# Performance work log

Measured on AMD Instinct MI355X. Metric: run time of the kernel, lower is better.

The kernel has to match this reference:

```python
import jax, jax.numpy as jnp
import numpy as np

N_HEAD = 16

def setup_inputs() -> dict:
    key = jax.random.key(0)
    ks = jax.random.split(key, 5)
    B, T, C = 2, 2048, 1024
    s = 0.02
    return {
        "x": jax.random.normal(ks[0], (B, T, C), jnp.float32),
        "W_attn": jax.random.normal(ks[1], (3 * C, C), jnp.float32) * s,
        "b_attn": jax.random.normal(ks[2], (3 * C,), jnp.float32) * s,
        "W_proj": jax.random.normal(ks[3], (C, C), jnp.float32) * s,
        "b_proj": jax.random.normal(ks[4], (C,), jnp.float32) * s,
    }

def reference(x, W_attn, b_attn, W_proj, b_proj):
    B, T, C = x.shape
    H = N_HEAD
    D = C // H
    # fused QKV projection (torch Linear: y = x @ W.T + b)
    qkv = jnp.einsum('btc,fc->btf', x, W_attn) + b_attn  # [B,T,3C]
    q, k, v = jnp.split(qkv, 3, axis=-1)
    def to_heads(t):
        return t.reshape(B, T, H, D).transpose(0, 2, 1, 3)  # [B,H,T,D]
    q, k, v = to_heads(q), to_heads(k), to_heads(v)
    scale = 1.0 / jnp.sqrt(jnp.array(D, x.dtype))
    scores = jnp.einsum('bhqd,bhkd->bhqk', q, k) * scale  # [B,H,T,T]
    causal = jnp.tril(jnp.ones((T, T), bool))
    scores = jnp.where(causal, scores, jnp.finfo(x.dtype).min)
    p = jax.nn.softmax(scores, axis=-1)
    y = jnp.einsum('bhqk,bhkd->bhqd', p, v)  # [B,H,T,D]
    y = y.transpose(0, 2, 1, 3).reshape(B, T, C)
    out = jnp.einsum('btc,oc->bto', y, W_proj) + b_proj
    return out
```

## Files before the change

### kernel.cpp

```cpp
#include <hip/hip_runtime.h>

typedef unsigned int u32;
typedef unsigned short u16;
typedef __attribute__((ext_vector_type(8))) short bf16x8;
typedef __attribute__((ext_vector_type(4))) float f32x4;
typedef __attribute__((ext_vector_type(16))) float f32x16;

#define T_ 2048
#define HEADS 16
#define DH 64

__device__ __forceinline__ u16 f2bf(float f) {
    union { float f; u32 u; } x; x.f = f;
    return (u16)((x.u + 0x7fffu + ((x.u >> 16) & 1u)) >> 16);
}
__device__ __forceinline__ u32 pkbf(float lo, float hi) {
    u32 r;
    asm("v_cvt_pk_bf16_f32 %0, %1, %2" : "=v"(r) : "v"(lo), "v"(hi));
    return r;
}
__device__ __forceinline__ void gll16(const void* g, void* l) {
    __builtin_amdgcn_global_load_lds(
        (const __attribute__((address_space(1))) void*)g,
        (__attribute__((address_space(3))) void*)l, 16, 0, 0);
}

#define QSCALE 0.18033688011112042f
#define DEFER_THR 8.0f

#define NG_X  (4096 * 128)
#define NG_WA (3072 * 128)
__global__ __launch_bounds__(256) void cvt_all(
    const float* __restrict__ x, const float* __restrict__ wa,
    const float* __restrict__ wp,
    u16* __restrict__ dx, u16* __restrict__ dwa, u16* __restrict__ dwp)
{
    int gid = blockIdx.x * 256 + threadIdx.x;
    const float* src; u16* dst;
    if (gid < NG_X)                { src = x;  dst = dx; }
    else if (gid < NG_X + NG_WA)   { src = wa; dst = dwa; gid -= NG_X; }
    else                           { src = wp; dst = dwp; gid -= NG_X + NG_WA; }
    const int m = gid >> 7, s = gid & 127;
    const int kt = s >> 3, seg = s & 7;
    const float4 a0 = *(const float4*)&src[m * 1024 + s * 8];
    const float4 a1 = *(const float4*)&src[m * 1024 + s * 8 + 4];
    uint4 t;
    t.x = pkbf(a0.x, a0.y); t.y = pkbf(a0.z, a0.w);
    t.z = pkbf(a1.x, a1.y); t.w = pkbf(a1.z, a1.w);
    const int mt = m >> 7, r = m & 127;
    char* d = (char*)dst + ((size_t)(mt * 16 + kt)) * 16384
              + r * 128 + ((seg ^ (r & 7)) << 4);
    *(uint4*)d = t;
}

template<int EPI>
__global__ __launch_bounds__(256, 3) void gemm_lds(
    const char* __restrict__ At, const char* __restrict__ Bt,
    const float* __restrict__ bias,
    u16* __restrict__ q, u16* __restrict__ k, u16* __restrict__ vt,
    float* __restrict__ outF)
{
    __shared__ __align__(16) char AsB[16384];
    __shared__ __align__(16) char BsB[16384];
    const int tid = threadIdx.x;
    const int l = tid & 63, li = l & 15, lg = l >> 4;
    const int w = tid >> 6, wm = w >> 1, wn = w & 1;
    const int m0 = blockIdx.y * 128, n0 = blockIdx.x * 128;
    const char* Ab = At + (size_t)blockIdx.y * (16 * 16384);
    const char* Bb = Bt + (size_t)blockIdx.x * (16 * 16384);

    f32x4 acc[4][4];
    #pragma unroll
    for (int i = 0; i < 4; ++i)
        #pragma unroll
        for (int j = 0; j < 4; ++j) acc[i][j] = (f32x4){0.f, 0.f, 0.f, 0.f};

    for (int kt = 0; kt < 16; ++kt) {
        const char* An = Ab + kt * 16384;
        const char* Bn = Bb + kt * 16384;
        #pragma unroll
        for (int i = 0; i < 4; ++i) {
            gll16(An + w * 4096 + i * 1024 + l * 16, &AsB[w * 4096 + i * 1024]);
            gll16(Bn + w * 4096 + i * 1024 + l * 16, &BsB[w * 4096 + i * 1024]);
        }
        asm volatile("s_waitcnt vmcnt(0)" ::: "memory");
        __syncthreads();
        #pragma unroll
        for (int kc = 0; kc < 2; ++kc) {
            const int key = ((kc * 4 + lg) ^ (li & 7)) << 4;
            bf16x8 a[4], b[4];
            #pragma unroll
            for (int f = 0; f < 4; ++f)
                a[f] = *(const bf16x8*)&AsB[(wm * 64 + f * 16 + li) * 128 + key];
            #pragma unroll
            for (int f = 0; f < 4; ++f)
                b[f] = *(const bf16x8*)&BsB[(wn * 64 + f * 16 + li) * 128 + key];
            #pragma unroll
            for (int mi = 0; mi < 4; ++mi)
                #pragma unroll
                for (int ni = 0; ni < 4; ++ni)
                    acc[mi][ni] = __builtin_amdgcn_mfma_f32_16x16x32_bf16(a[mi], b[ni], acc[mi][ni], 0, 0, 0);
        }
        __syncthreads();
    }

    const int mb = m0 + wm * 64;
    const int nb0 = n0 + wn * 64;
    if constexpr (EPI == 0) {
        const int part = n0 >> 10;
        if (part < 2) {
            u16* dst = (part == 0) ? q : k;
            const float scl = (part == 0) ? QSCALE : 1.0f;
            #pragma unroll
            for (int mi = 0; mi < 4; ++mi)
                #pragma unroll
                for (int r = 0; r < 4; ++r) {
                    const int m = mb + mi * 16 + lg * 4 + r;
                    const int bb = m >> 11, t = m & 2047;
                    #pragma unroll
                    for (int ni = 0; ni < 4; ++ni) {
                        const int n = nb0 + ni * 16 + li;
                        const int c = n & 1023;
                        const int h = c >> 6, d = c & 63;
                        const float val = (acc[mi][ni][r] + bias[n]) * scl;
                        dst[(((bb << 4) + h) * T_ + t) * DH + d] = f2bf(val);
                    }
                }
        } else {
            #pragma unroll
            for (int mi = 0; mi < 4; ++mi) {
                const int m = mb + mi * 16 + lg * 4;
                const int bb = m >> 11, t0 = m & 2047;
                #pragma unroll
                for (int ni = 0; ni < 4; ++ni) {
                    const int n = nb0 + ni * 16 + li;
                    const int c = n & 1023;
                    const int h = c >> 6, d = c & 63;
                    const float bz = bias[n];
                    u32 w0 = pkbf(acc[mi][ni][0] + bz, acc[mi][ni][1] + bz);
                    u32 w1 = pkbf(acc[mi][ni][2] + bz, acc[mi][ni][3] + bz);
                    *(uint2*)&vt[(((bb << 4) + h) * 64 + d) * (size_t)T_ + t0] = make_uint2(w0, w1);
                }
            }
        }
    } else {
        #pragma unroll
        for (int mi = 0; mi < 4; ++mi)
            #pragma unroll
            for (int r = 0; r < 4; ++r) {
                const int m = mb + mi * 16 + lg * 4 + r;
                #pragma unroll
                for (int ni = 0; ni < 4; ++ni) {
                    const int n = nb0 + ni * 16 + li;
                    outF[m * 1024 + n] = acc[mi][ni][r] + bias[n];
                }
            }
    }
}

__global__ __launch_bounds__(256, 2) void flash_attn(
    const u16* __restrict__ Q, const u16* __restrict__ K,
    const u16* __restrict__ Vt, char* __restrict__ Yt)
{
    __shared__ __align__(16) char KsB[2][8192];
    __shared__ __align__(16) char VsB[2][8192];
    __shared__ __align__(16) char PsB[4][4096];

    const int bh = blockIdx.x;
    const int px = blockIdx.y;
    const int tid = threadIdx.x;
    const int w  = tid >> 6;
    const int l  = tid & 63;
    const int q5 = l & 31, hi = l >> 5;
    const u16* Qb = Q  + (size_t)bh * (T_ * DH);
    const u16* Kb = K  + (size_t)bh * (T_ * DH);
    const u16* Vb = Vt + (size_t)bh * (T_ * DH);
    char* Pw = PsB[w];
    const int b = bh >> 4, h = bh & 15;

    const int myqt = (w < 2) ? px : (31 - px);
    const int wq0 = myqt * 64 + (w & 1) * 32;
    const int q_row = wq0 + q5;
    const int nb = 32 - px;

    const int srow = tid >> 3;
    const int sseg = tid & 7;
    const int skey0 = ((srow ^ (srow >> 3)) & 7) << 4;
    const int skey1 = ((srow ^ ((srow >> 3) + 4)) & 7) << 4;
    const int keyA0 = ((q5 ^ (q5 >> 3)) & 7) << 4;
    const int keyA1 = ((q5 ^ ((q5 >> 3) + 4)) & 7) << 4;
    const int pkey  = keyA0;

    bf16x8 qa[4];
    #pragma unroll
    for (int kd = 0; kd < 4; ++kd)
        qa[kd] = *(const bf16x8*)(Qb + q_row * 64 + kd * 16 + hi * 8);

    f32x16 o2[2];
    #pragma unroll
    for (int mf = 0; mf < 2; ++mf)
        #pragma unroll
        for (int r = 0; r < 16; ++r) o2[mf][r] = 0.f;
    float m_r = -INFINITY, l_r = 0.f;

    uint4 kr0, kr1, vr0, vr1;
    kr0 = *(const uint4*)(Kb + srow * 64 + sseg * 8);
    kr1 = *(const uint4*)(Kb + (srow + 32) * 64 + sseg * 8);
    vr0 = *(const uint4*)(Vb + (size_t)srow * T_ + sseg * 8);
    vr1 = *(const uint4*)(Vb + (size_t)(srow + 32) * T_ + sseg * 8);
    *(uint4*)&KsB[0][srow * 128        + ((sseg << 4) ^ skey0)] = kr0;
    *(uint4*)&KsB[0][(srow + 32) * 128 + ((sseg << 4) ^ skey1)] = kr1;
    *(uint4*)&VsB[0][srow * 128        + ((sseg << 4) ^ skey0)] = vr0;
    *(uint4*)&VsB[0][(srow + 32) * 128 + ((sseg << 4) ^ skey1)] = vr1;
    __syncthreads();

    for (int j = 0; j < nb; ++j) {
        const int cur = j & 1;
        const bool has_next = (j + 1 < nb);
        const bool act = (j <= myqt);
        if (has_next) {
            const int t0 = (j + 1) * 64;
            kr0 = *(const uint4*)(Kb + (t0 + srow) * 64 + sseg * 8);
            kr1 = *(const uint4*)(Kb + (t0 + srow + 32) * 64 + sseg * 8);
            vr0 = *(const uint4*)(Vb + (size_t)srow * T_ + t0 + sseg * 8);
            vr1 = *(const uint4*)(Vb + (size_t)(srow + 32) * T_ + t0 + sseg * 8);
        }
        f32x16 s2[2];
        if (act) {
            const char* Kc = KsB[cur];
            __builtin_amdgcn_s_setprio(1);
            #pragma unroll
            for (int mf = 0; mf < 2; ++mf) {
                #pragma unroll
                for (int r = 0; r < 16; ++r) s2[mf][r] = 0.f;
                const int rbase = (mf ? 32 : 0) + q5;
                const int ka = mf ? keyA1 : keyA0;
                #pragma unroll
                for (int kd = 0; kd < 4; ++kd) {
                    bf16x8 kb = *(const bf16x8*)&Kc[rbase * 128 + ((((2 * kd + hi) << 4)) ^ ka)];
                    s2[mf] = __builtin_amdgcn_mfma_f32_32x32x16_bf16(kb, qa[kd], s2[mf], 0, 0, 0);
                }
            }
            __builtin_amdgcn_s_setprio(0);
            if ((j + 1) * 64 > wq0) {
                const int kb0 = j * 64 + hi * 4;
                #pragma unroll
                for (int mf = 0; mf < 2; ++mf)
                    #pragma unroll
                    for (int r = 0; r < 16; ++r) {
                        const int kk = kb0 + (mf ? 32 : 0) + (r & 3) + ((r & 12) << 1);
                        if (kk > q_row) s2[mf][r] = -INFINITY;
                    }
            }
            float lm = s2[0][0];
            #pragma unroll
            for (int mf = 0; mf < 2; ++mf)
                #pragma unroll
                for (int r = 0; r < 16; ++r) lm = fmaxf(lm, s2[mf][r]);
            const float tm = fmaxf(lm, __shfl_xor(lm, 32));
            if (!__all(tm <= m_r + DEFER_THR)) {
                const float mnew = fmaxf(m_r, tm);
                const float corr = exp2f(m_r - mnew);
                m_r = mnew;
                l_r *= corr;
                #pragma unroll
                for (int mf = 0; mf < 2; ++mf)
                    #pragma unroll
                    for (int r = 0; r < 16; ++r) o2[mf][r] *= corr;
            }
            #pragma unroll
            for (int mf = 0; mf < 2; ++mf)
                #pragma unroll
                for (int m = 0; m < 4; ++m) {
                    const float p0 = exp2f(s2[mf][4 * m + 0] - m_r);
                    const float p1 = exp2f(s2[mf][4 * m + 1] - m_r);
                    const float p2 = exp2f(s2[mf][4 * m + 2] - m_r);
                    const float p3 = exp2f(s2[mf][4 * m + 3] - m_r);
                    l_r += (p0 + p1) + (p2 + p3);
                    uint2 pk = make_uint2(pkbf(p0, p1), pkbf(p2, p3));
                    *(uint2*)&Pw[q5 * 128 + ((((mf ? 4 : 0) + m) << 4) ^ pkey) + 8 * hi] = pk;
                }
        }
        if (has_next) {
            *(uint4*)&KsB[cur ^ 1][srow * 128        + ((sseg << 4) ^ skey0)] = kr0;
            *(uint4*)&KsB[cur ^ 1][(srow + 32) * 128 + ((sseg << 4) ^ skey1)] = kr1;
            *(uint4*)&VsB[cur ^ 1][srow * 128        + ((sseg << 4) ^ skey0)] = vr0;
            *(uint4*)&VsB[cur ^ 1][(srow + 32) * 128 + ((sseg << 4) ^ skey1)] = vr1;
        }
        if (act) {
            const char* Vc = VsB[cur];
            __builtin_amdgcn_s_setprio(1);
            #pragma unroll
            for (int ks = 0; ks < 4; ++ks) {
                bf16x8 pb = *(const bf16x8*)&Pw[q5 * 128 + (((2 * ks + hi) << 4) ^ pkey)];
                #pragma unroll
                for (int mf = 0; mf < 2; ++mf) {
                    const int rbase = (mf ? 32 : 0) + q5;
                    const int ka = mf ? keyA1 : keyA0;
                    bf16x8 va = *(const bf16x8*)&Vc[rbase * 128 + (((2 * ks + hi) << 4) ^ ka)];
                    o2[mf] = __builtin_amdgcn_mfma_f32_32x32x16_bf16(va, pb, o2[mf], 0, 0, 0);
                }
            }
            __builtin_amdgcn_s_setprio(0);
        }
        __syncthreads();
    }

    l_r += __shfl_xor(l_r, 32);
    const float inv = 1.0f / l_r;
    const int r128 = (myqt & 1) * 64 + (w & 1) * 32 + q5;
    const int rk = (r128 & 7) << 4;
    char* yrow = Yt + ((size_t)((b * 16 + (myqt >> 1)) * 16 + h)) * 16384 + r128 * 128;
    #pragma unroll
    for (int mf = 0; mf < 2; ++mf)
        #pragma unroll
        for (int m = 0; m < 4; ++m) {
            uint2 pk = make_uint2(
                pkbf(o2[mf][4 * m + 0] * inv, o2[mf][4 * m + 1] * inv),
                pkbf(o2[mf][4 * m + 2] * inv, o2[mf][4 * m + 3] * inv));
            *(uint2*)&yrow[((((mf ? 4 : 0) + m) << 4) ^ rk) + 8 * hi] = pk;
        }
}

extern "C" void kernel_launch(void* const* d_in, const int* in_sizes, int n_in,
                              void* d_out, int out_size, void* d_ws, size_t ws_size,
                              hipStream_t stream) {
    const float* x      = (const float*)d_in[0];
    const float* W_attn = (const float*)d_in[1];
    const float* b_attn = (const float*)d_in[2];
    const float* W_proj = (const float*)d_in[3];
    const float* b_proj = (const float*)d_in[4];
    float* out = (float*)d_out;

    char* ws = (char*)d_ws;
    u16* q   = (u16*)ws;
    u16* k   = (u16*)(ws + (8u << 20));
    u16* vt  = (u16*)(ws + (16u << 20));
    char* xb = ws + (24u << 20);
    char* wab = ws + (32u << 20);
    char* wpb = ws + (38u << 20);

    cvt_all<<<4096, 256, 0, stream>>>(x, W_attn, W_proj, (u16*)xb, (u16*)wab, (u16*)wpb);
    gemm_lds<0><<<dim3(24, 32), 256, 0, stream>>>(xb, wab, b_attn, q, k, vt, nullptr);
    flash_attn<<<dim3(32, 16), 256, 0, stream>>>(q, k, vt, xb );
    gemm_lds<1><<<dim3(8, 32), 256, 0, stream>>>(xb , wpb, b_proj,
                                                 nullptr, nullptr, nullptr, out);
}
```

Baseline: 121.5 us.

## Split paired-query-tile attention blocks into single-tile 128-thread blocks

```diff
diff --git a/kernel.cpp b/kernel.cpp
--- a/kernel.cpp
+++ b/kernel.cpp
@@ -158,16 +158,17 @@
     }
 }
 
-__global__ __launch_bounds__(256, 2) void flash_attn(
+__global__ __launch_bounds__(128, 2) void flash_attn(
     const u16* __restrict__ Q, const u16* __restrict__ K,
     const u16* __restrict__ Vt, char* __restrict__ Yt)
 {
     __shared__ __align__(16) char KsB[2][8192];
     __shared__ __align__(16) char VsB[2][8192];
-    __shared__ __align__(16) char PsB[4][4096];
+    __shared__ __align__(16) char PsB[2][4096];
 
     const int bh = blockIdx.x;
-    const int px = blockIdx.y;
+    const int slot = blockIdx.y;
+    const int qt = (slot & 1) ? (31 - (slot >> 1)) : (slot >> 1);
     const int tid = threadIdx.x;
     const int w  = tid >> 6;
     const int l  = tid & 63;
@@ -178,13 +179,12 @@
     char* Pw = PsB[w];
     const int b = bh >> 4, h = bh & 15;
 
-    const int myqt = (w < 2) ? px : (31 - px);
-    const int wq0 = myqt * 64 + (w & 1) * 32;
+    const int wq0 = qt * 64 + w * 32;
     const int q_row = wq0 + q5;
-    const int nb = 32 - px;
-
-    const int srow = tid >> 3;
-    const int sseg = tid & 7;
+    const int nkv = qt + 1;
+
+    const int srow = tid >> 2;
+    const int sseg = tid & 3;
     const int skey0 = ((srow ^ (srow >> 3)) & 7) << 4;
     const int skey1 = ((srow ^ ((srow >> 3) + 4)) & 7) << 4;
     const int keyA0 = ((q5 ^ (q5 >> 3)) & 7) << 4;
@@ -203,114 +203,125 @@
         for (int r = 0; r < 16; ++r) o2[mf][r] = 0.f;
     float m_r = -INFINITY, l_r = 0.f;
 
-    uint4 kr0, kr1, vr0, vr1;
+    uint4 kr0, kr1, kr2, kr3, vr0, vr1, vr2, vr3;
     kr0 = *(const uint4*)(Kb + srow * 64 + sseg * 8);
-    kr1 = *(const uint4*)(Kb + (srow + 32) * 64 + sseg * 8);
+    kr1 = *(const uint4*)(Kb + srow * 64 + (sseg + 4) * 8);
+    kr2 = *(const uint4*)(Kb + (srow + 32) * 64 + sseg * 8);
+    kr3 = *(const uint4*)(Kb + (srow + 32) * 64 + (sseg + 4) * 8);
     vr0 = *(const uint4*)(Vb + (size_t)srow * T_ + sseg * 8);
-    vr1 = *(const uint4*)(Vb + (size_t)(srow + 32) * T_ + sseg * 8);
-    *(uint4*)&KsB[0][srow * 128        + ((sseg << 4) ^ skey0)] = kr0;
-    *(uint4*)&KsB[0][(srow + 32) * 128 + ((sseg << 4) ^ skey1)] = kr1;
-    *(uint4*)&VsB[0][srow * 128        + ((sseg << 4) ^ skey0)] = vr0;
-    *(uint4*)&VsB[0][(srow + 32) * 128 + ((sseg << 4) ^ skey1)] = vr1;
+    vr1 = *(const uint4*)(Vb + (size_t)srow * T_ + (sseg + 4) * 8);
+    vr2 = *(const uint4*)(Vb + (size_t)(srow + 32) * T_ + sseg * 8);
+    vr3 = *(const uint4*)(Vb + (size_t)(srow + 32) * T_ + (sseg + 4) * 8);
+    *(uint4*)&KsB[0][srow * 128        + ((sseg       << 4) ^ skey0)] = kr0;
+    *(uint4*)&KsB[0][srow * 128        + (((sseg + 4) << 4) ^ skey0)] = kr1;
+    *(uint4*)&KsB[0][(srow + 32) * 128 + ((sseg       << 4) ^ skey1)] = kr2;
+    *(uint4*)&KsB[0][(srow + 32) * 128 + (((sseg + 4) << 4) ^ skey1)] = kr3;
+    *(uint4*)&VsB[0][srow * 128        + ((sseg       << 4) ^ skey0)] = vr0;
+    *(uint4*)&VsB[0][srow * 128        + (((sseg + 4) << 4) ^ skey0)] = vr1;
+    *(uint4*)&VsB[0][(srow + 32) * 128 + ((sseg       << 4) ^ skey1)] = vr2;
+    *(uint4*)&VsB[0][(srow + 32) * 128 + (((sseg + 4) << 4) ^ skey1)] = vr3;
     __syncthreads();
 
-    for (int j = 0; j < nb; ++j) {
+    for (int j = 0; j < nkv; ++j) {
         const int cur = j & 1;
-        const bool has_next = (j + 1 < nb);
-        const bool act = (j <= myqt);
+        const bool has_next = (j + 1 < nkv);
         if (has_next) {
             const int t0 = (j + 1) * 64;
             kr0 = *(const uint4*)(Kb + (t0 + srow) * 64 + sseg * 8);
-            kr1 = *(const uint4*)(Kb + (t0 + srow + 32) * 64 + sseg * 8);
+            kr1 = *(const uint4*)(Kb + (t0 + srow) * 64 + (sseg + 4) * 8);
+            kr2 = *(const uint4*)(Kb + (t0 + srow + 32) * 64 + sseg * 8);
+            kr3 = *(const uint4*)(Kb + (t0 + srow + 32) * 64 + (sseg + 4) * 8);
             vr0 = *(const uint4*)(Vb + (size_t)srow * T_ + t0 + sseg * 8);
-            vr1 = *(const uint4*)(Vb + (size_t)(srow + 32) * T_ + t0 + sseg * 8);
-        }
+            vr1 = *(const uint4*)(Vb + (size_t)srow * T_ + t0 + (sseg + 4) * 8);
+            vr2 = *(const uint4*)(Vb + (size_t)(srow + 32) * T_ + t0 + sseg * 8);
+            vr3 = *(const uint4*)(Vb + (size_t)(srow + 32) * T_ + t0 + (sseg + 4) * 8);
+        }
+        const char* Kc = KsB[cur];
         f32x16 s2[2];
-        if (act) {
-            const char* Kc = KsB[cur];
-            __builtin_amdgcn_s_setprio(1);
+        __builtin_amdgcn_s_setprio(1);
+        #pragma unroll
+        for (int mf = 0; mf < 2; ++mf) {
+            #pragma unroll
+            for (int r = 0; r < 16; ++r) s2[mf][r] = 0.f;
+            const int rbase = (mf ? 32 : 0) + q5;
+            const int ka = mf ? keyA1 : keyA0;
+            #pragma unroll
+            for (int kd = 0; kd < 4; ++kd) {
+                bf16x8 kb = *(const bf16x8*)&Kc[rbase * 128 + (((2 * kd + hi) << 4) ^ ka)];
+                s2[mf] = __builtin_amdgcn_mfma_f32_32x32x16_bf16(kb, qa[kd], s2[mf], 0, 0, 0);
+            }
+        }
+        __builtin_amdgcn_s_setprio(0);
+        if ((j + 1) * 64 > wq0) {
+            const int kb0 = j * 64 + hi * 4;
+            #pragma unroll
+            for (int mf = 0; mf < 2; ++mf)
+                #pragma unroll
+                for (int r = 0; r < 16; ++r) {
+                    const int kk = kb0 + (mf ? 32 : 0) + (r & 3) + ((r & 12) << 1);
+                    if (kk > q_row) s2[mf][r] = -INFINITY;
+                }
+        }
+        float lm = s2[0][0];
+        #pragma unroll
+        for (int mf = 0; mf < 2; ++mf)
+            #pragma unroll
+            for (int r = 0; r < 16; ++r) lm = fmaxf(lm, s2[mf][r]);
+        const float tm = fmaxf(lm, __shfl_xor(lm, 32));
+        if (!__all(tm <= m_r + DEFER_THR)) {
+            const float mnew = fmaxf(m_r, tm);
+            const float corr = exp2f(m_r - mnew);
+            m_r = mnew;
+            l_r *= corr;
+            #pragma unroll
+            for (int mf = 0; mf < 2; ++mf)
+                #pragma unroll
+                for (int r = 0; r < 16; ++r) o2[mf][r] *= corr;
+        }
+        #pragma unroll
+        for (int mf = 0; mf < 2; ++mf)
+            #pragma unroll
+            for (int m = 0; m < 4; ++m) {
+                const float p0 = exp2f(s2[mf][4 * m + 0] - m_r);
+                const float p1 = exp2f(s2[mf][4 * m + 1] - m_r);
+                const float p2 = exp2f(s2[mf][4 * m + 2] - m_r);
+                const float p3 = exp2f(s2[mf][4 * m + 3] - m_r);
+                l_r += (p0 + p1) + (p2 + p3);
+                uint2 pk = make_uint2(pkbf(p0, p1), pkbf(p2, p3));
+                *(uint2*)&Pw[q5 * 128 + ((((mf ? 4 : 0) + m) << 4) ^ pkey) + 8 * hi] = pk;
+            }
+        if (has_next) {
+            *(uint4*)&KsB[cur ^ 1][srow * 128        + ((sseg       << 4) ^ skey0)] = kr0;
+            *(uint4*)&KsB[cur ^ 1][srow * 128        + (((sseg + 4) << 4) ^ skey0)] = kr1;
+            *(uint4*)&KsB[cur ^ 1][(srow + 32) * 128 + ((sseg       << 4) ^ skey1)] = kr2;
+            *(uint4*)&KsB[cur ^ 1][(srow + 32) * 128 + (((sseg + 4) << 4) ^ skey1)] = kr3;
+            *(uint4*)&VsB[cur ^ 1][srow * 128        + ((sseg       << 4) ^ skey0)] = vr0;
+            *(uint4*)&VsB[cur ^ 1][srow * 128        + (((sseg + 4) << 4) ^ skey0)] = vr1;
+            *(uint4*)&VsB[cur ^ 1][(srow + 32) * 128 + ((sseg       << 4) ^ skey1)] = vr2;
+            *(uint4*)&VsB[cur ^ 1][(srow + 32) * 128 + (((sseg + 4) << 4) ^ skey1)] = vr3;
+        }
+        const char* Vc = VsB[cur];
+        __builtin_amdgcn_s_setprio(1);
+        #pragma unroll
+        for (int ks = 0; ks < 4; ++ks) {
+            bf16x8 pb = *(const bf16x8*)&Pw[q5 * 128 + (((2 * ks + hi) << 4) ^ pkey)];
             #pragma unroll
             for (int mf = 0; mf < 2; ++mf) {
-                #pragma unroll
-                for (int r = 0; r < 16; ++r) s2[mf][r] = 0.f;
                 const int rbase = (mf ? 32 : 0) + q5;
                 const int ka = mf ? keyA1 : keyA0;
-                #pragma unroll
-                for (int kd = 0; kd < 4; ++kd) {
-                    bf16x8 kb = *(const bf16x8*)&Kc[rbase * 128 + ((((2 * kd + hi) << 4)) ^ ka)];
-                    s2[mf] = __builtin_amdgcn_mfma_f32_32x32x16_bf16(kb, qa[kd], s2[mf], 0, 0, 0);
-                }
-            }
-            __builtin_amdgcn_s_setprio(0);
-            if ((j + 1) * 64 > wq0) {
-                const int kb0 = j * 64 + hi * 4;
-                #pragma unroll
-                for (int mf = 0; mf < 2; ++mf)
-                    #pragma unroll
-                    for (int r = 0; r < 16; ++r) {
-                        const int kk = kb0 + (mf ? 32 : 0) + (r & 3) + ((r & 12) << 1);
-                        if (kk > q_row) s2[mf][r] = -INFINITY;
-                    }
-            }
-            float lm = s2[0][0];
-            #pragma unroll
-            for (int mf = 0; mf < 2; ++mf)
-                #pragma unroll
-                for (int r = 0; r < 16; ++r) lm = fmaxf(lm, s2[mf][r]);
-            const float tm = fmaxf(lm, __shfl_xor(lm, 32));
-            if (!__all(tm <= m_r + DEFER_THR)) {
-                const float mnew = fmaxf(m_r, tm);
-                const float corr = exp2f(m_r - mnew);
-                m_r = mnew;
-                l_r *= corr;
-                #pragma unroll
-                for (int mf = 0; mf < 2; ++mf)
-                    #pragma unroll
-                    for (int r = 0; r < 16; ++r) o2[mf][r] *= corr;
-            }
-            #pragma unroll
-            for (int mf = 0; mf < 2; ++mf)
-                #pragma unroll
-                for (int m = 0; m < 4; ++m) {
-                    const float p0 = exp2f(s2[mf][4 * m + 0] - m_r);
-                    const float p1 = exp2f(s2[mf][4 * m + 1] - m_r);
-                    const float p2 = exp2f(s2[mf][4 * m + 2] - m_r);
-                    const float p3 = exp2f(s2[mf][4 * m + 3] - m_r);
-                    l_r += (p0 + p1) + (p2 + p3);
-                    uint2 pk = make_uint2(pkbf(p0, p1), pkbf(p2, p3));
-                    *(uint2*)&Pw[q5 * 128 + ((((mf ? 4 : 0) + m) << 4) ^ pkey) + 8 * hi] = pk;
-                }
-        }
-        if (has_next) {
-            *(uint4*)&KsB[cur ^ 1][srow * 128        + ((sseg << 4) ^ skey0)] = kr0;
-            *(uint4*)&KsB[cur ^ 1][(srow + 32) * 128 + ((sseg << 4) ^ skey1)] = kr1;
-            *(uint4*)&VsB[cur ^ 1][srow * 128        + ((sseg << 4) ^ skey0)] = vr0;
-            *(uint4*)&VsB[cur ^ 1][(srow + 32) * 128 + ((sseg << 4) ^ skey1)] = vr1;
-        }
-        if (act) {
-            const char* Vc = VsB[cur];
-            __builtin_amdgcn_s_setprio(1);
-            #pragma unroll
-            for (int ks = 0; ks < 4; ++ks) {
-                bf16x8 pb = *(const bf16x8*)&Pw[q5 * 128 + (((2 * ks + hi) << 4) ^ pkey)];
-                #pragma unroll
-                for (int mf = 0; mf < 2; ++mf) {
-                    const int rbase = (mf ? 32 : 0) + q5;
-                    const int ka = mf ? keyA1 : keyA0;
-                    bf16x8 va = *(const bf16x8*)&Vc[rbase * 128 + (((2 * ks + hi) << 4) ^ ka)];
-                    o2[mf] = __builtin_amdgcn_mfma_f32_32x32x16_bf16(va, pb, o2[mf], 0, 0, 0);
-                }
-            }
-            __builtin_amdgcn_s_setprio(0);
-        }
+                bf16x8 va = *(const bf16x8*)&Vc[rbase * 128 + (((2 * ks + hi) << 4) ^ ka)];
+                o2[mf] = __builtin_amdgcn_mfma_f32_32x32x16_bf16(va, pb, o2[mf], 0, 0, 0);
+            }
+        }
+        __builtin_amdgcn_s_setprio(0);
         __syncthreads();
     }
 
     l_r += __shfl_xor(l_r, 32);
     const float inv = 1.0f / l_r;
-    const int r128 = (myqt & 1) * 64 + (w & 1) * 32 + q5;
+    const int r128 = (qt & 1) * 64 + w * 32 + q5;
     const int rk = (r128 & 7) << 4;
-    char* yrow = Yt + ((size_t)((b * 16 + (myqt >> 1)) * 16 + h)) * 16384 + r128 * 128;
+    char* yrow = Yt + ((size_t)((b * 16 + (qt >> 1)) * 16 + h)) * 16384 + r128 * 128;
     #pragma unroll
     for (int mf = 0; mf < 2; ++mf)
         #pragma unroll
@@ -342,7 +353,7 @@
 
     cvt_all<<<4096, 256, 0, stream>>>(x, W_attn, W_proj, (u16*)xb, (u16*)wab, (u16*)wpb);
     gemm_lds<0><<<dim3(24, 32), 256, 0, stream>>>(xb, wab, b_attn, q, k, vt, nullptr);
-    flash_attn<<<dim3(32, 16), 256, 0, stream>>>(q, k, vt, xb );
+    flash_attn<<<dim3(32, 32), 128, 0, stream>>>(q, k, vt, xb );
     gemm_lds<1><<<dim3(8, 32), 256, 0, stream>>>(xb , wpb, b_proj,
                                                  nullptr, nullptr, nullptr, out);
 }
```

Measured after the change: 120.8 us. Within noise of the previous version (-0.6%).
